# Kernel optimization log

Hardware: AMD Instinct MI355X
Metric: run time of the kernel (lower is better)

The kernel has to match this reference:

```python
import jax, jax.numpy as jnp
import numpy as np
from jax import lax

B, J, C, K, TOK, CH, H = 2048, 17, 480, 3, 64, 960, 6
HD = C // H  # 80
EPS = 1e-5

def gelu(x):
    return jax.nn.gelu(x, approximate=False)

def layernorm(x, g, b):
    mu = jnp.mean(x, axis=-1, keepdims=True)
    var = jnp.var(x, axis=-1, keepdims=True)
    return (x - mu) * lax.rsqrt(var + EPS) * g + b

def groupnorm(x, g, b, groups=16):
    # x: (B, C, J) -> normalize over (C//groups * J) per group
    n, c, j = x.shape
    xg = x.reshape(n, groups, -1)
    mu = jnp.mean(xg, axis=-1, keepdims=True)
    var = jnp.var(xg, axis=-1, keepdims=True)
    xg = (xg - mu) * lax.rsqrt(var + EPS)
    return xg.reshape(n, c, j) * g[None, :, None] + b[None, :, None]

def dwconv1d(x, w, b, pad):
    # x: (B, C, J), w: (C, 1, Kw) depthwise
    y = lax.conv_general_dilated(x, w, window_strides=(1,), padding=[(pad, pad)],
                                 dimension_numbers=('NCH', 'OIH', 'NCH'),
                                 feature_group_count=x.shape[1])
    return y + b[None, :, None]

def setup_inputs() -> dict:
    key = jax.random.key(0)
    ks = jax.random.split(key, 16)
    n = jax.random.normal
    return {
        'x': n(ks[0], (B, J, C), dtype=jnp.float32),
        'adj': n(ks[1], (K, J, J), dtype=jnp.float32) * 0.1,
        'norm1_g': jnp.ones((J,), jnp.float32), 'norm1_b': jnp.zeros((J,), jnp.float32),
        'gcn1_w': n(ks[2], (C * K, C), jnp.float32) * 0.02, 'gcn1_b': jnp.zeros((C * K,), jnp.float32),
        'dw_w': n(ks[3], (C, 1, 7), jnp.float32) * 0.1, 'dw_b': jnp.zeros((C,), jnp.float32),
        'dwgn_g': jnp.ones((C,), jnp.float32), 'dwgn_b': jnp.zeros((C,), jnp.float32),
        'mlp1_w1': n(ks[4], (TOK, J), jnp.float32) * 0.02, 'mlp1_b1': jnp.zeros((TOK,), jnp.float32),
        'mlp1_w2': n(ks[5], (J, TOK), jnp.float32) * 0.02, 'mlp1_b2': jnp.zeros((J,), jnp.float32),
        'qkv_w': n(ks[6], (3 * C, C), jnp.float32) * 0.02, 'qkv_b': jnp.zeros((3 * C,), jnp.float32),
        'proj_w': n(ks[7], (C, C), jnp.float32) * 0.02, 'proj_b': jnp.zeros((C,), jnp.float32),
        'pos_w': n(ks[8], (C, 1, 9), jnp.float32) * 0.1, 'pos_b': jnp.zeros((C,), jnp.float32),
        'gnf_g': jnp.ones((C,), jnp.float32), 'gnf_b': jnp.zeros((C,), jnp.float32),
        'norm2_g': jnp.ones((C,), jnp.float32), 'norm2_b': jnp.zeros((C,), jnp.float32),
        'gcn2_w': n(ks[9], (C * K, C), jnp.float32) * 0.02, 'gcn2_b': jnp.zeros((C * K,), jnp.float32),
        'mlp2_w1': n(ks[10], (CH, C), jnp.float32) * 0.02, 'mlp2_b1': jnp.zeros((CH,), jnp.float32),
        'mlp2_w2': n(ks[11], (C, CH), jnp.float32) * 0.02, 'mlp2_b2': jnp.zeros((C,), jnp.float32),
    }

def reference(x, adj, norm1_g, norm1_b, gcn1_w, gcn1_b, dw_w, dw_b, dwgn_g, dwgn_b,
              mlp1_w1, mlp1_b1, mlp1_w2, mlp1_b2, qkv_w, qkv_b, proj_w, proj_b,
              pos_w, pos_b, gnf_g, gnf_b, norm2_g, norm2_b, gcn2_w, gcn2_b,
              mlp2_w1, mlp2_b1, mlp2_w2, mlp2_b2):
    b = x.shape[0]
    xc = jnp.transpose(x, (0, 2, 1))            # (b, c, j)
    res_spatial = xc
    xn = layernorm(xc, norm1_g, norm1_b)        # LN over joints
    # --- GCN branch 1: 1x1 conv then adjacency einsum ---
    y = jnp.einsum('bcj,oc->boj', xn, gcn1_w) + gcn1_b[None, :, None]
    y = y.reshape(b, K, C, J)
    x_gcn1 = jnp.einsum('bkcv,kvw->bcw', y, adj)  # (b, c, j)
    # --- depthwise conv + GN + GELU + token Mlp ---
    d = gelu(groupnorm(dwconv1d(xn, dw_w, dw_b, 3), dwgn_g, dwgn_b))
    x_mjem = gelu(d @ mlp1_w1.T + mlp1_b1) @ mlp1_w2.T + mlp1_b2  # mix over j
    # --- spatial global attention (6 heads over joints + dwconv pos) ---
    xt = jnp.transpose(xn, (0, 2, 1))           # (b, j, c)
    qkv = xt @ qkv_w.T + qkv_b                  # (b, j, 3c)
    qkv = qkv.reshape(b, J, 3, H, HD).transpose(2, 0, 3, 1, 4)  # (3, b, h, j, hd)
    q, k, v = qkv[0], qkv[1], qkv[2]
    attn = jax.nn.softmax(jnp.einsum('bhqd,bhkd->bhqk', q, k) * (HD ** -0.5), axis=-1)
    o = jnp.einsum('bhqk,bhkd->bhqd', attn, v).transpose(0, 2, 1, 3).reshape(b, J, C)
    o = o @ proj_w.T + proj_b
    x_gsa = jnp.transpose(o, (0, 2, 1)) + dwconv1d(xn, pos_w, pos_b, 4)  # (b, c, j)
    # --- fuse ---
    fused = groupnorm(x_gsa + x_gcn1 + x_mjem, gnf_g, gnf_b)
    xc = res_spatial + gelu(fused)
    # --- channel stage ---
    xj = jnp.transpose(xc, (0, 2, 1))           # (b, j, c)
    res_channel = xj
    xn2 = layernorm(xj, norm2_g, norm2_b)       # LN over channels
    xcc = jnp.transpose(xn2, (0, 2, 1))         # (b, c, j)
    y2 = jnp.einsum('bcj,oc->boj', xcc, gcn2_w) + gcn2_b[None, :, None]
    y2 = y2.reshape(b, K, C, J)
    x_gcn2 = jnp.transpose(jnp.einsum('bkcv,kvw->bcw', y2, adj), (0, 2, 1))  # (b, j, c)
    mlp_out = gelu(xn2 @ mlp2_w1.T + mlp2_b1) @ mlp2_w2.T + mlp2_b2
    # sca_block is undefined in the source __init__ -> identity
    return res_channel + mlp_out + x_gcn2
```

## Files before the change

kernel.cpp:

```cpp
#include <hip/hip_runtime.h>
#include <hip/hip_bf16.h>

#define DI __device__ __forceinline__

typedef __attribute__((ext_vector_type(8))) short bf16x8;
typedef __attribute__((ext_vector_type(4))) float f32x4;

namespace {
constexpr int B_ = 2048, J_ = 17, C_ = 480, K_ = 3, TOK_ = 64, CH_ = 960, H_ = 6, HD_ = 80;
constexpr int C3_ = 3 * C_;
constexpr float EPSF = 1e-5f;
}

DI float gelu_f(float x) {
  const float kA2 = 2.f * 0.7978845608028654f;
  const float kB2 = 2.f * 0.7978845608028654f * 0.044715f;
  const float z = fmaf(-kB2 * x, x * x, -kA2 * x);
  return x / (1.f + __expf(z));
}
DI float b2f(__hip_bfloat16 v) { return __bfloat162float(v); }
DI __hip_bfloat16 f2b(float v) { return __float2bfloat16(v); }
DI float s2f(short s) { return __uint_as_float(((unsigned)(unsigned short)s) << 16); }
DI unsigned pk2(float a, float b) {
  union { unsigned u; __hip_bfloat16 h[2]; } p;
  p.h[0] = f2b(a); p.h[1] = f2b(b);
  return p.u;
}

DI void gl16(const void* g, void* l) {
  __builtin_amdgcn_global_load_lds(
      (const __attribute__((address_space(1))) unsigned int*)g,
      (__attribute__((address_space(3))) unsigned int*)l, 16, 0, 0);
}

__global__ __launch_bounds__(256) void cvt_all_kernel(
    const float* __restrict__ s0, const float* __restrict__ s1,
    const float* __restrict__ s2, const float* __restrict__ s3,
    const float* __restrict__ s4, const float* __restrict__ s5,
    __hip_bfloat16* __restrict__ d) {
  constexpr int SG = C3_ * C_;
  constexpr int O1 = SG, O2 = 2 * SG, O3 = 3 * SG;
  constexpr int O4 = O3 + C_ * C_;
  constexpr int O5 = O4 + CH_ * C_;
  const int i = (blockIdx.x * 256 + threadIdx.x) * 4;
  const float* s; int off;
  if      (i < O1) { s = s0; off = i; }
  else if (i < O2) { s = s1; off = i - O1; }
  else if (i < O3) { s = s2; off = i - O2; }
  else if (i < O4) { s = s3; off = i - O3; }
  else if (i < O5) { s = s4; off = i - O4; }
  else             { s = s5; off = i - O5; }
  const float4 v = *reinterpret_cast<const float4*>(s + off);
  union { ushort4 u; __hip_bfloat16 h[4]; } o;
  o.h[0] = f2b(v.x); o.h[1] = f2b(v.y); o.h[2] = f2b(v.z); o.h[3] = f2b(v.w);
  *reinterpret_cast<ushort4*>(reinterpret_cast<unsigned short*>(d) + i) = o.u;
}

__global__ __launch_bounds__(256) void ln1_kernel(const float* __restrict__ x,
                                                  const float* __restrict__ g,
                                                  const float* __restrict__ bt,
                                                  __hip_bfloat16* __restrict__ xnT, int nBC) {
  const int t = blockIdx.x * 256 + threadIdx.x;
  if (t >= nBC) return;
  const int b = t / C_, c = t % C_;
  const float* xp = x + (size_t)b * J_ * C_ + c;
  float v[J_];
  float s = 0.f;
  #pragma unroll
  for (int j = 0; j < J_; ++j) { v[j] = xp[j * C_]; s += v[j]; }
  const float mu = s * (1.f / J_);
  float sq = 0.f;
  #pragma unroll
  for (int j = 0; j < J_; ++j) { const float d = v[j] - mu; sq += d * d; }
  const float rs = rsqrtf(sq * (1.f / J_) + EPSF);
  __hip_bfloat16* op = xnT + (size_t)b * J_ * C_ + c;
  #pragma unroll
  for (int j = 0; j < J_; ++j) op[j * C_] = f2b((v[j] - mu) * rs * g[j] + bt[j]);
}

template<int KD, int EPI>
__global__ __launch_bounds__(512) void gemm_lds(const __hip_bfloat16* __restrict__ A,
                                                const __hip_bfloat16* __restrict__ W,
                                                const float* __restrict__ bias,
                                                __hip_bfloat16* __restrict__ Dst, int Ntot,
                                                const __hip_bfloat16* __restrict__ r1,
                                                const __hip_bfloat16* __restrict__ r2,
                                                float* __restrict__ outf) {
  constexpr int NST = (KD + 63) / 64;
  constexpr bool TAIL = (KD % 64) != 0;
  constexpr int ROWB = KD * 2;
  __shared__ __align__(16) char smem[28672];

  const int lane = threadIdx.x & 63;
  const int wid  = threadIdx.x >> 6;
  const int m0g = blockIdx.x * 128;
  const int n0g = blockIdx.y * 96;

  const int srow = lane >> 3;
  const int scbs = ((lane & 7) * 16) ^ ((srow & 7) << 4);
  auto stage = [&](int t) {
    const int kb = t * 128;
    #pragma unroll
    for (int i = wid; i < 28; i += 8) {
      if (i < 16) {
        const int r = i * 8 + srow;
        gl16((const char*)A + (size_t)(m0g + r) * ROWB + kb + scbs, smem + i * 1024);
      } else {
        const int r = (i - 16) * 8 + srow;
        gl16((const char*)W + (size_t)(n0g + r) * ROWB + kb + scbs, smem + 16384 + (i - 16) * 1024);
      }
    }
  };

  const f32x4 zf = {0.f, 0.f, 0.f, 0.f};
  f32x4 acc[2][3];
  #pragma unroll
  for (int mi = 0; mi < 2; ++mi)
    #pragma unroll
    for (int ni = 0; ni < 3; ++ni) acc[mi][ni] = zf;

  const int rA0 = (wid >> 1) * 32 + (lane & 15);
  const int rB0 = (wid & 1) * 48 + (lane & 15);
  const int swz = (lane & 7) << 4;
  const int kq  = (lane >> 4) * 16;

  for (int t = 0; t < NST; ++t) {
    stage(t);
    __syncthreads();
    const int nks = (TAIL && t == NST - 1) ? 1 : 2;
    for (int ks = 0; ks < nks; ++ks) {
      const int cb = (ks * 64 + kq) ^ swz;
      bf16x8 av[2], bv[3];
      #pragma unroll
      for (int mi = 0; mi < 2; ++mi)
        av[mi] = *reinterpret_cast<const bf16x8*>(smem + (rA0 + mi * 16) * 128 + cb);
      #pragma unroll
      for (int ni = 0; ni < 3; ++ni)
        bv[ni] = *reinterpret_cast<const bf16x8*>(smem + 16384 + (rB0 + ni * 16) * 128 + cb);
      #pragma unroll
      for (int mi = 0; mi < 2; ++mi)
        #pragma unroll
        for (int ni = 0; ni < 3; ++ni)
          acc[mi][ni] = __builtin_amdgcn_mfma_f32_16x16x32_bf16(av[mi], bv[ni], acc[mi][ni], 0, 0, 0);
    }
    __syncthreads();
  }

  const int lc0 = (wid & 1) * 48 + (lane & 15);
  const int lr0 = (wid >> 1) * 32 + ((lane >> 4) << 2);
  if (EPI == 2) {
    #pragma unroll
    for (int ni = 0; ni < 3; ++ni) {
      const int col = n0g + lc0 + ni * 16;
      const float bvv = bias[col];
      #pragma unroll
      for (int mi = 0; mi < 2; ++mi) {
        #pragma unroll
        for (int r = 0; r < 4; ++r) {
          const size_t idx = (size_t)(m0g + lr0 + mi * 16 + r) * Ntot + col;
          outf[idx] = acc[mi][ni][r] + bvv + b2f(r1[idx]) + b2f(r2[idx]);
        }
      }
    }
  } else {
    __hip_bfloat16* ct = (__hip_bfloat16*)smem;
    #pragma unroll
    for (int ni = 0; ni < 3; ++ni) {
      const float bvv = bias[n0g + lc0 + ni * 16];
      #pragma unroll
      for (int mi = 0; mi < 2; ++mi) {
        #pragma unroll
        for (int r = 0; r < 4; ++r) {
          float v = acc[mi][ni][r] + bvv;
          if (EPI == 1) v = gelu_f(v);
          ct[(lr0 + mi * 16 + r) * 104 + lc0 + ni * 16] = f2b(v);
        }
      }
    }
    __syncthreads();
    const int tid = threadIdx.x;
    #pragma unroll
    for (int it = 0; it < 3; ++it) {
      const int idx = it * 512 + tid;
      const int row = idx / 12, s = idx - row * 12;
      const uint4 v = *(const uint4*)(smem + row * 208 + s * 16);
      *(uint4*)((char*)Dst + ((size_t)(m0g + row) * Ntot + n0g) * 2 + s * 16) = v;
    }
  }
}

__global__ __launch_bounds__(512) void attn_kernel(const __hip_bfloat16* __restrict__ qkv,
                                                   __hip_bfloat16* __restrict__ o) {
  constexpr int SROW = 1448;
  const int b = blockIdx.x, tid = threadIdx.x;
  __shared__ __align__(16) __hip_bfloat16 sqkv[J_ * SROW];
  __shared__ float S[H_][J_][J_];
  {
    const uint4* src = (const uint4*)(qkv + (size_t)b * J_ * C3_);
    uint4* dst = (uint4*)&sqkv[0];
    for (int i = tid; i < 3060; i += 512) {
      const int j = i / 180, u = i - j * 180;
      dst[j * 181 + u] = src[i];
    }
  }
  __syncthreads();
  for (int i = tid; i < H_ * J_ * J_; i += 512) {
    const int h = i / (J_ * J_), r = i % (J_ * J_), qj = r / J_, kj = r % J_;
    const bf16x8* qp = (const bf16x8*)&sqkv[qj * SROW + h * HD_];
    const bf16x8* kp = (const bf16x8*)&sqkv[kj * SROW + C_ + h * HD_];
    float acc = 0.f;
    #pragma unroll
    for (int d8 = 0; d8 < HD_ / 8; ++d8) {
      const bf16x8 qv = qp[d8], kv = kp[d8];
      #pragma unroll
      for (int t = 0; t < 8; ++t) acc += s2f(qv[t]) * s2f(kv[t]);
    }
    S[h][qj][kj] = acc * 0.11180339887498949f;
  }
  __syncthreads();
  if (tid < H_ * J_) {
    const int h = tid / J_, qj = tid % J_;
    float* row = S[h][qj];
    float m = row[0];
    #pragma unroll
    for (int kk = 1; kk < J_; ++kk) m = fmaxf(m, row[kk]);
    float s = 0.f;
    #pragma unroll
    for (int kk = 0; kk < J_; ++kk) { const float e = __expf(row[kk] - m); row[kk] = e; s += e; }
    const float inv = 1.f / s;
    #pragma unroll
    for (int kk = 0; kk < J_; ++kk) row[kk] *= inv;
  }
  __syncthreads();
  __hip_bfloat16* ob = o + (size_t)b * J_ * C_;
  for (int i = tid; i < J_ * C_; i += 512) {
    const int qj = i / C_, c = i % C_;
    const int h = c / HD_;
    const float* srow = S[h][qj];
    float acc = 0.f;
    #pragma unroll
    for (int kk = 0; kk < J_; ++kk) acc += srow[kk] * b2f(sqkv[kk * SROW + 2 * C_ + c]);
    ob[i] = f2b(acc);
  }
}

__global__ __launch_bounds__(512) void gcn_contract_kernel(const __hip_bfloat16* __restrict__ y,
                                                           const float* __restrict__ adj,
                                                           __hip_bfloat16* __restrict__ g) {
  const int b = blockIdx.x, tid = threadIdx.x;
  __shared__ float adjl[K_ * J_ * J_];
  for (int i = tid; i < K_ * J_ * J_; i += 512) adjl[i] = adj[i];
  __syncthreads();
  const int c = tid;
  if (c < C_) {
    float yv[K_][J_];
    const __hip_bfloat16* yb = y + (size_t)b * J_ * C3_ + c;
    #pragma unroll
    for (int k = 0; k < K_; ++k)
      #pragma unroll
      for (int v = 0; v < J_; ++v)
        yv[k][v] = b2f(yb[(size_t)v * C3_ + k * C_]);
    __hip_bfloat16* gp = g + (size_t)b * J_ * C_ + c;
    #pragma unroll
    for (int w = 0; w < J_; ++w) {
      float acc = 0.f;
      #pragma unroll
      for (int k = 0; k < K_; ++k)
        #pragma unroll
        for (int v = 0; v < J_; ++v)
          acc += yv[k][v] * adjl[(k * J_ + v) * J_ + w];
      gp[w * C_] = f2b(acc);
    }
  }
}

__global__ __launch_bounds__(512) void dwconv_kernel(const __hip_bfloat16* __restrict__ xnT,
    const float* __restrict__ dww, const float* __restrict__ dwb,
    const float* __restrict__ gg, const float* __restrict__ gb,
    __hip_bfloat16* __restrict__ dpr) {
  __shared__ __align__(16) __hip_bfloat16 xl[J_ * C_];
  __shared__ float gstat[16][2];
  const int b = blockIdx.x, tid = threadIdx.x;
  {
    const uint4* src = (const uint4*)(xnT + (size_t)b * J_ * C_);
    uint4* dst = (uint4*)&xl[0];
    for (int i = tid; i < 1020; i += 512) dst[i] = src[i];
  }
  if (tid < 32) gstat[tid >> 1][tid & 1] = 0.f;
  __syncthreads();
  const int c = tid;
  float dv[J_];
  if (c < C_) {
    float xv[J_];
    #pragma unroll
    for (int j = 0; j < J_; ++j) xv[j] = b2f(xl[j * C_ + c]);
    float wv[7];
    #pragma unroll
    for (int t = 0; t < 7; ++t) wv[t] = dww[c * 7 + t];
    const float bias = dwb[c];
    float s = 0.f, sqs = 0.f;
    #pragma unroll
    for (int j = 0; j < J_; ++j) {
      float acc = bias;
      #pragma unroll
      for (int t = 0; t < 7; ++t) {
        const int jj = j - 3 + t;
        if (jj >= 0 && jj < J_) acc = fmaf(xv[jj], wv[t], acc);
      }
      dv[j] = acc; s += acc; sqs += acc * acc;
    }
    atomicAdd(&gstat[c / 30][0], s);
    atomicAdd(&gstat[c / 30][1], sqs);
  }
  __syncthreads();
// ... 55 lines not shown
    #pragma unroll
    for (int kk = 0; kk < 2; ++kk)
      a2[mi][kk] = *(const bf16x8*)(lds + W2P + (lr + mi * 16) * 144 + kk * 64 + kc * 16);
  float b1v[4][4];
  #pragma unroll
  for (int mi = 0; mi < 4; ++mi)
    #pragma unroll
    for (int r = 0; r < 4; ++r) b1v[mi][r] = b1[mi * 16 + kc * 4 + r];
  float b2v[4];
  #pragma unroll
  for (int r = 0; r < 4; ++r) b2v[r] = b2[kc * 4 + r];
  const float b2v16 = b2[16];

  char* hs = lds + HS + wid * 2304;
  const f32x4 zf4 = {0.f, 0.f, 0.f, 0.f};
  #pragma unroll
  for (int it = 0; it < 4; ++it) {
    const int gcb = blockIdx.x * 16 + wid * 4 + it;
    const int b = gcb / 30, cbl = gcb - b * 30;
    const size_t row0 = (size_t)b * C_ + cbl * 16;
    const bf16x8 bf = *(const bf16x8*)(dpr + (row0 + lr) * 32 + kc * 8);
    f32x4 acc1[4];
    #pragma unroll
    for (int mi = 0; mi < 4; ++mi)
      acc1[mi] = __builtin_amdgcn_mfma_f32_16x16x32_bf16(a1[mi], bf, zf4, 0, 0, 0);
    #pragma unroll
    for (int mi = 0; mi < 4; ++mi) {
      const float g0 = gelu_f(acc1[mi][0] + b1v[mi][0]);
      const float g1 = gelu_f(acc1[mi][1] + b1v[mi][1]);
      const float g2 = gelu_f(acc1[mi][2] + b1v[mi][2]);
      const float g3 = gelu_f(acc1[mi][3] + b1v[mi][3]);
      unsigned* hp = (unsigned*)(hs + lr * 144 + (mi * 16 + kc * 4) * 2);
      hp[0] = pk2(g0, g1);
      hp[1] = pk2(g2, g3);
    }
    f32x4 acc2[2] = {zf4, zf4};
    #pragma unroll
    for (int kk = 0; kk < 2; ++kk) {
      const bf16x8 hb = *(const bf16x8*)(hs + lr * 144 + kk * 64 + kc * 16);
      #pragma unroll
      for (int mi = 0; mi < 2; ++mi)
        acc2[mi] = __builtin_amdgcn_mfma_f32_16x16x32_bf16(a2[mi][kk], hb, acc2[mi], 0, 0, 0);
    }
    __hip_bfloat16* mp = mjem_r + (row0 + lr) * 20;
    #pragma unroll
    for (int r = 0; r < 4; ++r)
      mp[kc * 4 + r] = f2b(acc2[0][r] + b2v[r]);
    if (kc == 0) mp[16] = f2b(acc2[1][0] + b2v16);
  }
}

__global__ __launch_bounds__(512) void fuse_kernel(
    const float* __restrict__ x, const __hip_bfloat16* __restrict__ xnT,
    const __hip_bfloat16* __restrict__ g1o, const __hip_bfloat16* __restrict__ projo,
    const __hip_bfloat16* __restrict__ mjem_r,
    const float* __restrict__ posw, const float* __restrict__ posb,
    const float* __restrict__ gnfg, const float* __restrict__ gnfb,
    const float* __restrict__ n2g, const float* __restrict__ n2b,
    __hip_bfloat16* __restrict__ resch, __hip_bfloat16* __restrict__ xn2) {
  const int b = blockIdx.x, tid = threadIdx.x;
  __shared__ float xcl[J_][C_];
  __shared__ float gstat[16][2];
  __shared__ float lnst[J_][2];
  if (tid < 32) gstat[tid >> 1][tid & 1] = 0.f;
  __syncthreads();
  const int c = tid;
  float fz[J_];
  if (c < C_) {
    float xnv[J_];
    const __hip_bfloat16* xp = xnT + (size_t)b * J_ * C_ + c;
    #pragma unroll
    for (int j = 0; j < J_; ++j) xnv[j] = b2f(xp[j * C_]);
    float pw[9];
    #pragma unroll
    for (int t = 0; t < 9; ++t) pw[t] = posw[c * 9 + t];
    const float pb = posb[c];
    const __hip_bfloat16* pj = projo + (size_t)b * J_ * C_ + c;
    const __hip_bfloat16* mp = mjem_r + ((size_t)b * C_ + c) * 20;
    const __hip_bfloat16* gp = g1o + (size_t)b * J_ * C_ + c;
    float s = 0.f, sqs = 0.f;
    #pragma unroll
    for (int j = 0; j < J_; ++j) {
      float pos = pb;
      #pragma unroll
      for (int t = 0; t < 9; ++t) {
        const int jj = j - 4 + t;
        if (jj >= 0 && jj < J_) pos += xnv[jj] * pw[t];
      }
      const float f = b2f(pj[j * C_]) + pos + b2f(gp[j * C_]) + b2f(mp[j]);
      fz[j] = f; s += f; sqs += f * f;
    }
    atomicAdd(&gstat[c / 30][0], s);
    atomicAdd(&gstat[c / 30][1], sqs);
  }
  __syncthreads();
  if (c < C_) {
    const float mu = gstat[c / 30][0] * (1.f / 510.f);
    const float var = gstat[c / 30][1] * (1.f / 510.f) - mu * mu;
    const float rs = rsqrtf(var + EPSF);
    const float sc = gnfg[c], of = gnfb[c];
    const float* xr = x + (size_t)b * J_ * C_ + c;
    __hip_bfloat16* rp = resch + (size_t)b * J_ * C_ + c;
    #pragma unroll
    for (int j = 0; j < J_; ++j) {
      const float xcv = xr[j * C_] + gelu_f((fz[j] - mu) * rs * sc + of);
      xcl[j][c] = xcv;
      rp[j * C_] = f2b(xcv);
    }
  }
  __syncthreads();
  const int wid = tid >> 6, lane = tid & 63;
  for (int j = wid; j < J_; j += 8) {
    float ls = 0.f, lq = 0.f;
    for (int cc = lane; cc < C_; cc += 64) { const float v = xcl[j][cc]; ls += v; lq += v * v; }
    #pragma unroll
    for (int off = 32; off > 0; off >>= 1) { ls += __shfl_xor(ls, off); lq += __shfl_xor(lq, off); }
    if (lane == 0) {
      const float mu = ls * (1.f / C_);
      const float var = lq * (1.f / C_) - mu * mu;
      lnst[j][0] = mu; lnst[j][1] = rsqrtf(var + EPSF);
    }
  }
  __syncthreads();
  if (c < C_) {
    const float sc = n2g[c], of = n2b[c];
    __hip_bfloat16* xp2 = xn2 + (size_t)b * J_ * C_ + c;
    #pragma unroll
    for (int j = 0; j < J_; ++j)
      xp2[j * C_] = f2b((xcl[j][c] - lnst[j][0]) * lnst[j][1] * sc + of);
  }
}

extern "C" void kernel_launch(void* const* d_in, const int* in_sizes, int n_in,
                              void* d_out, int out_size, void* d_ws, size_t ws_size,
                              hipStream_t stream) {
  const float* x      = (const float*)d_in[0];
  const float* adj    = (const float*)d_in[1];
  const float* n1g    = (const float*)d_in[2];
  const float* n1b    = (const float*)d_in[3];
  const float* gcn1_w = (const float*)d_in[4];
  const float* gcn1_b = (const float*)d_in[5];
  const float* dw_w   = (const float*)d_in[6];
  const float* dw_b   = (const float*)d_in[7];
  const float* dwgn_g = (const float*)d_in[8];
  const float* dwgn_b = (const float*)d_in[9];
  const float* m1w1   = (const float*)d_in[10];
  const float* m1b1   = (const float*)d_in[11];
  const float* m1w2   = (const float*)d_in[12];
  const float* m1b2   = (const float*)d_in[13];
  const float* qkv_w  = (const float*)d_in[14];
  const float* qkv_b  = (const float*)d_in[15];
  const float* proj_w = (const float*)d_in[16];
  const float* proj_b = (const float*)d_in[17];
  const float* pos_w  = (const float*)d_in[18];
  const float* pos_b  = (const float*)d_in[19];
  const float* gnf_g  = (const float*)d_in[20];
  const float* gnf_b  = (const float*)d_in[21];
  const float* n2g    = (const float*)d_in[22];
  const float* n2b    = (const float*)d_in[23];
  const float* gcn2_w = (const float*)d_in[24];
  const float* gcn2_b = (const float*)d_in[25];
  const float* m2w1   = (const float*)d_in[26];
  const float* m2b1   = (const float*)d_in[27];
  const float* m2w2   = (const float*)d_in[28];
  const float* m2b2   = (const float*)d_in[29];
  float* out = (float*)d_out;
  char* ws = (char*)d_ws;
  (void)in_sizes; (void)n_in; (void)out_size;

  auto a256 = [](size_t b) { return (b + 255) & ~(size_t)255; };
  const size_t wbytes = 3 * a256((size_t)C3_ * C_ * 2) + a256((size_t)C_ * C_ * 2) +
                        a256((size_t)CH_ * C_ * 2) + a256((size_t)C_ * CH_ * 2);
  int nch = 16;
  for (int cand : {1, 2, 4, 8, 16}) {
    const size_t Bcb = (size_t)(B_ / cand);
    const size_t Mcb = Bcb * J_;
    const size_t fp = wbytes + a256(Mcb * C3_ * 2) + 5 * a256(Mcb * C_ * 2) +
                      a256(Bcb * C_ * 20 * 2) + a256(Bcb * C_ * 32 * 2);
    if (fp <= ws_size) { nch = cand; break; }
  }
  const int Bc = B_ / nch;
  const int Mc = Bc * J_;

  size_t off = 0;
  auto alloc = [&](size_t bytes) { char* p = ws + off; off += a256(bytes); return p; };
  __hip_bfloat16* w_qkv = (__hip_bfloat16*)alloc((size_t)C3_ * C_ * 2);
  __hip_bfloat16* w_g1  = (__hip_bfloat16*)alloc((size_t)C3_ * C_ * 2);
  __hip_bfloat16* w_g2  = (__hip_bfloat16*)alloc((size_t)C3_ * C_ * 2);
  __hip_bfloat16* w_pr  = (__hip_bfloat16*)alloc((size_t)C_ * C_ * 2);
  __hip_bfloat16* w_21  = (__hip_bfloat16*)alloc((size_t)CH_ * C_ * 2);
  __hip_bfloat16* w_22  = (__hip_bfloat16*)alloc((size_t)C_ * CH_ * 2);
  __hip_bfloat16* BIG   = (__hip_bfloat16*)alloc((size_t)Mc * C3_ * 2);
  __hip_bfloat16* xnT   = (__hip_bfloat16*)alloc((size_t)Mc * C_ * 2);
  __hip_bfloat16* attno = (__hip_bfloat16*)alloc((size_t)Mc * C_ * 2);
  __hip_bfloat16* projo = (__hip_bfloat16*)alloc((size_t)Mc * C_ * 2);
  __hip_bfloat16* g1o   = (__hip_bfloat16*)alloc((size_t)Mc * C_ * 2);
  __hip_bfloat16* resch = (__hip_bfloat16*)alloc((size_t)Mc * C_ * 2);
  __hip_bfloat16* mjemr = (__hip_bfloat16*)alloc((size_t)Bc * C_ * 20 * 2);
  __hip_bfloat16* dpr   = (__hip_bfloat16*)alloc((size_t)Bc * C_ * 32 * 2);
  __hip_bfloat16* xn2   = attno;
  __hip_bfloat16* g2o   = g1o;
  __hip_bfloat16* hbuf  = BIG;

  cvt_all_kernel<<<3150, 256, 0, stream>>>(qkv_w, gcn1_w, gcn2_w, proj_w, m2w1, m2w2, w_qkv);

  for (int ci = 0; ci < nch; ++ci) {
    const float* xc = x + (size_t)ci * Bc * J_ * C_;
    float* outc = out + (size_t)ci * Bc * J_ * C_;
    ln1_kernel<<<(Bc * C_ + 255) / 256, 256, 0, stream>>>(xc, n1g, n1b, xnT, Bc * C_);
    gemm_lds<C_, 0><<<dim3(Mc / 128, C3_ / 96), 512, 0, stream>>>(xnT, w_qkv, qkv_b, BIG, C3_, nullptr, nullptr, nullptr);
    attn_kernel<<<Bc, 512, 0, stream>>>(BIG, attno);
    gemm_lds<C_, 0><<<dim3(Mc / 128, C3_ / 96), 512, 0, stream>>>(xnT, w_g1, gcn1_b, BIG, C3_, nullptr, nullptr, nullptr);
    gcn_contract_kernel<<<Bc, 512, 0, stream>>>(BIG, adj, g1o);
    gemm_lds<C_, 0><<<dim3(Mc / 128, C_ / 96), 512, 0, stream>>>(attno, w_pr, proj_b, projo, C_, nullptr, nullptr, nullptr);
    dwconv_kernel<<<Bc, 512, 0, stream>>>(xnT, dw_w, dw_b, dwgn_g, dwgn_b, dpr);
    mlp_kernel<<<Bc * 30 / 16, 256, 0, stream>>>(dpr, m1w1, m1b1, m1w2, m1b2, mjemr);
    fuse_kernel<<<Bc, 512, 0, stream>>>(xc, xnT, g1o, projo, mjemr, pos_w, pos_b,
                                        gnf_g, gnf_b, n2g, n2b, resch, xn2);
    gemm_lds<C_, 0><<<dim3(Mc / 128, C3_ / 96), 512, 0, stream>>>(xn2, w_g2, gcn2_b, BIG, C3_, nullptr, nullptr, nullptr);
    gcn_contract_kernel<<<Bc, 512, 0, stream>>>(BIG, adj, g2o);
    gemm_lds<C_, 1><<<dim3(Mc / 128, CH_ / 96), 512, 0, stream>>>(xn2, w_21, m2b1, hbuf, CH_, nullptr, nullptr, nullptr);
    gemm_lds<CH_, 2><<<dim3(Mc / 128, C_ / 96), 512, 0, stream>>>(hbuf, w_22, m2b2, nullptr, C_, resch, g2o, outc);
  }
}
```

Before: 735.4 us.

## Switch GEMM tiles to 128x128 with padded N dimensions

Changes the GEMM block tile from 128x96 to 128x128, giving each wave a 4x2 MFMA subtile. Weights and intermediate buffers are zero-padded to multiples of 128 columns (1536, 1024, 512), and the consumer kernels are updated to the new strides. This improves operand reuse per LDS read and reduces A-tile refetch across blocks. The cost is extra padded MFMA work and a larger LDS footprint.

```diff
diff --git a/kernel.cpp b/kernel.cpp
--- a/kernel.cpp
+++ b/kernel.cpp
@@ -9,6 +9,7 @@
 namespace {
 constexpr int B_ = 2048, J_ = 17, C_ = 480, K_ = 3, TOK_ = 64, CH_ = 960, H_ = 6, HD_ = 80;
 constexpr int C3_ = 3 * C_;
+constexpr int C3P_ = 1536, CHP_ = 1024, CP_ = 512;
 constexpr float EPSF = 1e-5f;
 }
 
@@ -33,26 +34,20 @@
       (__attribute__((address_space(3))) unsigned int*)l, 16, 0, 0);
 }
 
-__global__ __launch_bounds__(256) void cvt_all_kernel(
-    const float* __restrict__ s0, const float* __restrict__ s1,
-    const float* __restrict__ s2, const float* __restrict__ s3,
-    const float* __restrict__ s4, const float* __restrict__ s5,
-    __hip_bfloat16* __restrict__ d) {
-  constexpr int SG = C3_ * C_;
-  constexpr int O1 = SG, O2 = 2 * SG, O3 = 3 * SG;
-  constexpr int O4 = O3 + C_ * C_;
-  constexpr int O5 = O4 + CH_ * C_;
-  const int i = (blockIdx.x * 256 + threadIdx.x) * 4;
-  const float* s; int off;
-  if      (i < O1) { s = s0; off = i; }
-  else if (i < O2) { s = s1; off = i - O1; }
-  else if (i < O3) { s = s2; off = i - O2; }
-  else if (i < O4) { s = s3; off = i - O3; }
-  else if (i < O5) { s = s4; off = i - O4; }
-  else             { s = s5; off = i - O5; }
-  const float4 v = *reinterpret_cast<const float4*>(s + off);
+__global__ __launch_bounds__(256) void cvt_pad_kernel(const float* __restrict__ s,
+                                                      __hip_bfloat16* __restrict__ d,
+                                                      int Nlog, int Kd, int n4) {
+  const int q = blockIdx.x * 256 + threadIdx.x;
+  if (q >= n4) return;
+  const int i = q * 4;
+  const int row = i / Kd, col = i - row * Kd;
   union { ushort4 u; __hip_bfloat16 h[4]; } o;
-  o.h[0] = f2b(v.x); o.h[1] = f2b(v.y); o.h[2] = f2b(v.z); o.h[3] = f2b(v.w);
+  if (row < Nlog) {
+    const float4 v = *reinterpret_cast<const float4*>(s + (size_t)row * Kd + col);
+    o.h[0] = f2b(v.x); o.h[1] = f2b(v.y); o.h[2] = f2b(v.z); o.h[3] = f2b(v.w);
+  } else {
+    o.h[0] = f2b(0.f); o.h[1] = f2b(0.f); o.h[2] = f2b(0.f); o.h[3] = f2b(0.f);
+  }
   *reinterpret_cast<ushort4*>(reinterpret_cast<unsigned short*>(d) + i) = o.u;
 }
 
@@ -78,49 +73,51 @@
   for (int j = 0; j < J_; ++j) op[j * C_] = f2b((v[j] - mu) * rs * g[j] + bt[j]);
 }
 
-template<int KD, int EPI>
+template<int KD, int LDA, int EPI>
 __global__ __launch_bounds__(512) void gemm_lds(const __hip_bfloat16* __restrict__ A,
                                                 const __hip_bfloat16* __restrict__ W,
                                                 const float* __restrict__ bias,
-                                                __hip_bfloat16* __restrict__ Dst, int Ntot,
+                                                __hip_bfloat16* __restrict__ Dst,
+                                                int NP, int Nlog,
                                                 const __hip_bfloat16* __restrict__ r1,
                                                 const __hip_bfloat16* __restrict__ r2,
                                                 float* __restrict__ outf) {
   constexpr int NST = (KD + 63) / 64;
   constexpr bool TAIL = (KD % 64) != 0;
-  constexpr int ROWB = KD * 2;
-  __shared__ __align__(16) char smem[28672];
+  constexpr int AROWB = LDA * 2;
+  constexpr int WROWB = KD * 2;
+  __shared__ __align__(16) char smem[34816];
 
   const int lane = threadIdx.x & 63;
   const int wid  = threadIdx.x >> 6;
   const int m0g = blockIdx.x * 128;
-  const int n0g = blockIdx.y * 96;
+  const int n0g = blockIdx.y * 128;
 
   const int srow = lane >> 3;
   const int scbs = ((lane & 7) * 16) ^ ((srow & 7) << 4);
   auto stage = [&](int t) {
     const int kb = t * 128;
     #pragma unroll
-    for (int i = wid; i < 28; i += 8) {
+    for (int i = wid; i < 32; i += 8) {
       if (i < 16) {
         const int r = i * 8 + srow;
-        gl16((const char*)A + (size_t)(m0g + r) * ROWB + kb + scbs, smem + i * 1024);
+        gl16((const char*)A + (size_t)(m0g + r) * AROWB + kb + scbs, smem + i * 1024);
       } else {
         const int r = (i - 16) * 8 + srow;
-        gl16((const char*)W + (size_t)(n0g + r) * ROWB + kb + scbs, smem + 16384 + (i - 16) * 1024);
+        gl16((const char*)W + (size_t)(n0g + r) * WROWB + kb + scbs, smem + 16384 + (i - 16) * 1024);
       }
     }
   };
 
   const f32x4 zf = {0.f, 0.f, 0.f, 0.f};
-  f32x4 acc[2][3];
-  #pragma unroll
-  for (int mi = 0; mi < 2; ++mi)
-    #pragma unroll
-    for (int ni = 0; ni < 3; ++ni) acc[mi][ni] = zf;
-
-  const int rA0 = (wid >> 1) * 32 + (lane & 15);
-  const int rB0 = (wid & 1) * 48 + (lane & 15);
+  f32x4 acc[4][2];
+  #pragma unroll
+  for (int mi = 0; mi < 4; ++mi)
+    #pragma unroll
+    for (int ni = 0; ni < 2; ++ni) acc[mi][ni] = zf;
+
+  const int rA0 = (wid >> 2) * 64 + (lane & 15);
+  const int rB0 = (wid & 3) * 32 + (lane & 15);
   const int swz = (lane & 7) << 4;
   const int kq  = (lane >> 4) * 16;
 
@@ -130,61 +127,64 @@
     const int nks = (TAIL && t == NST - 1) ? 1 : 2;
     for (int ks = 0; ks < nks; ++ks) {
       const int cb = (ks * 64 + kq) ^ swz;
-      bf16x8 av[2], bv[3];
-      #pragma unroll
-      for (int mi = 0; mi < 2; ++mi)
+      bf16x8 av[4], bv[2];
+      #pragma unroll
+      for (int mi = 0; mi < 4; ++mi)
         av[mi] = *reinterpret_cast<const bf16x8*>(smem + (rA0 + mi * 16) * 128 + cb);
       #pragma unroll
-      for (int ni = 0; ni < 3; ++ni)
+      for (int ni = 0; ni < 2; ++ni)
         bv[ni] = *reinterpret_cast<const bf16x8*>(smem + 16384 + (rB0 + ni * 16) * 128 + cb);
       #pragma unroll
-      for (int mi = 0; mi < 2; ++mi)
+      for (int mi = 0; mi < 4; ++mi)
         #pragma unroll
-        for (int ni = 0; ni < 3; ++ni)
+        for (int ni = 0; ni < 2; ++ni)
           acc[mi][ni] = __builtin_amdgcn_mfma_f32_16x16x32_bf16(av[mi], bv[ni], acc[mi][ni], 0, 0, 0);
     }
     __syncthreads();
   }
 
-  const int lc0 = (wid & 1) * 48 + (lane & 15);
-  const int lr0 = (wid >> 1) * 32 + ((lane >> 4) << 2);
+  const int lc0 = (wid & 3) * 32 + (lane & 15);
+  const int lr0 = (wid >> 2) * 64 + ((lane >> 4) << 2);
   if (EPI == 2) {
     #pragma unroll
-    for (int ni = 0; ni < 3; ++ni) {
+    for (int ni = 0; ni < 2; ++ni) {
       const int col = n0g + lc0 + ni * 16;
-      const float bvv = bias[col];
-      #pragma unroll
-      for (int mi = 0; mi < 2; ++mi) {
+      if (col < Nlog) {
+        const float bvv = bias[col];
         #pragma unroll
-        for (int r = 0; r < 4; ++r) {
-          const size_t idx = (size_t)(m0g + lr0 + mi * 16 + r) * Ntot + col;
-          outf[idx] = acc[mi][ni][r] + bvv + b2f(r1[idx]) + b2f(r2[idx]);
+        for (int mi = 0; mi < 4; ++mi) {
+          #pragma unroll
+          for (int r = 0; r < 4; ++r) {
+            const size_t idx = (size_t)(m0g + lr0 + mi * 16 + r) * Nlog + col;
+            outf[idx] = acc[mi][ni][r] + bvv + b2f(r1[idx]) + b2f(r2[idx]);
+          }
         }
       }
     }
   } else {
     __hip_bfloat16* ct = (__hip_bfloat16*)smem;
     #pragma unroll
-    for (int ni = 0; ni < 3; ++ni) {
-      const float bvv = bias[n0g + lc0 + ni * 16];
-      #pragma unroll
-      for (int mi = 0; mi < 2; ++mi) {
+    for (int ni = 0; ni < 2; ++ni) {
+      const int col = n0g + lc0 + ni * 16;
+      const float bvv = (col < Nlog) ? bias[col] : 0.f;
+      #pragma unroll
+      for (int mi = 0; mi < 4; ++mi) {
         #pragma unroll
         for (int r = 0; r < 4; ++r) {
           float v = acc[mi][ni][r] + bvv;
           if (EPI == 1) v = gelu_f(v);
-          ct[(lr0 + mi * 16 + r) * 104 + lc0 + ni * 16] = f2b(v);
+          ct[(lr0 + mi * 16 + r) * 136 + lc0 + ni * 16] = f2b(v);
         }
       }
     }
     __syncthreads();
     const int tid = threadIdx.x;
     #pragma unroll
-    for (int it = 0; it < 3; ++it) {
+    for (int it = 0; it < 4; ++it) {
       const int idx = it * 512 + tid;
-      const int row = idx / 12, s = idx - row * 12;
-      const uint4 v = *(const uint4*)(smem + row * 208 + s * 16);
-      *(uint4*)((char*)Dst + ((size_t)(m0g + row) * Ntot + n0g) * 2 + s * 16) = v;
+      const int row = idx >> 4, s = idx & 15;
+      const uint4 v = *(const uint4*)(smem + row * 272 + s * 16);
+      *(uint4*)((char*)Dst + ((size_t)(m0g + row) * NP + n0g) * 2 + s * 16) = v;
     }
   }
 }
@@ -196,11 +196,11 @@
   __shared__ __align__(16) __hip_bfloat16 sqkv[J_ * SROW];
   __shared__ float S[H_][J_][J_];
   {
-    const uint4* src = (const uint4*)(qkv + (size_t)b * J_ * C3_);
+    const uint4* src = (const uint4*)(qkv + (size_t)b * J_ * C3P_);
     uint4* dst = (uint4*)&sqkv[0];
     for (int i = tid; i < 3060; i += 512) {
       const int j = i / 180, u = i - j * 180;
-      dst[j * 181 + u] = src[i];
+      dst[j * 181 + u] = src[j * 192 + u];
     }
   }
   __syncthreads();
@@ -254,12 +254,12 @@
   const int c = tid;
   if (c < C_) {
     float yv[K_][J_];
-    const __hip_bfloat16* yb = y + (size_t)b * J_ * C3_ + c;
+    const __hip_bfloat16* yb = y + (size_t)b * J_ * C3P_ + c;
     #pragma unroll
     for (int k = 0; k < K_; ++k)
       #pragma unroll
       for (int v = 0; v < J_; ++v)
-        yv[k][v] = b2f(yb[(size_t)v * C3_ + k * C_]);
+        yv[k][v] = b2f(yb[(size_t)v * C3P_ + k * C_]);
     __hip_bfloat16* gp = g + (size_t)b * J_ * C_ + c;
     #pragma unroll
     for (int w = 0; w < J_; ++w) {
@@ -444,7 +444,7 @@
     #pragma unroll
     for (int t = 0; t < 9; ++t) pw[t] = posw[c * 9 + t];
     const float pb = posb[c];
-    const __hip_bfloat16* pj = projo + (size_t)b * J_ * C_ + c;
+    const __hip_bfloat16* pj = projo + (size_t)b * J_ * CP_ + c;
     const __hip_bfloat16* mp = mjem_r + ((size_t)b * C_ + c) * 20;
     const __hip_bfloat16* gp = g1o + (size_t)b * J_ * C_ + c;
     float s = 0.f, sqs = 0.f;
@@ -456,7 +456,7 @@
         const int jj = j - 4 + t;
         if (jj >= 0 && jj < J_) pos += xnv[jj] * pw[t];
       }
-      const float f = b2f(pj[j * C_]) + pos + b2f(gp[j * C_]) + b2f(mp[j]);
+      const float f = b2f(pj[j * CP_]) + pos + b2f(gp[j * C_]) + b2f(mp[j]);
       fz[j] = f; s += f; sqs += f * f;
     }
     atomicAdd(&gstat[c / 30][0], s);
@@ -538,13 +538,14 @@
   (void)in_sizes; (void)n_in; (void)out_size;
 
   auto a256 = [](size_t b) { return (b + 255) & ~(size_t)255; };
-  const size_t wbytes = 3 * a256((size_t)C3_ * C_ * 2) + a256((size_t)C_ * C_ * 2) +
-                        a256((size_t)CH_ * C_ * 2) + a256((size_t)C_ * CH_ * 2);
+  const size_t wbytes = 3 * a256((size_t)C3P_ * C_ * 2) + a256((size_t)CP_ * C_ * 2) +
+                        a256((size_t)CHP_ * C_ * 2) + a256((size_t)CP_ * CH_ * 2);
   int nch = 16;
   for (int cand : {1, 2, 4, 8, 16}) {
     const size_t Bcb = (size_t)(B_ / cand);
     const size_t Mcb = Bcb * J_;
-    const size_t fp = wbytes + a256(Mcb * C3_ * 2) + 5 * a256(Mcb * C_ * 2) +
+    const size_t fp = wbytes + a256(Mcb * C3P_ * 2) + a256(Mcb * CP_ * 2) +
+                      4 * a256(Mcb * C_ * 2) +
                       a256(Bcb * C_ * 20 * 2) + a256(Bcb * C_ * 32 * 2);
     if (fp <= ws_size) { nch = cand; break; }
   }
@@ -553,16 +554,16 @@
 
   size_t off = 0;
   auto alloc = [&](size_t bytes) { char* p = ws + off; off += a256(bytes); return p; };
-  __hip_bfloat16* w_qkv = (__hip_bfloat16*)alloc((size_t)C3_ * C_ * 2);
-  __hip_bfloat16* w_g1  = (__hip_bfloat16*)alloc((size_t)C3_ * C_ * 2);
-  __hip_bfloat16* w_g2  = (__hip_bfloat16*)alloc((size_t)C3_ * C_ * 2);
-  __hip_bfloat16* w_pr  = (__hip_bfloat16*)alloc((size_t)C_ * C_ * 2);
-  __hip_bfloat16* w_21  = (__hip_bfloat16*)alloc((size_t)CH_ * C_ * 2);
-  __hip_bfloat16* w_22  = (__hip_bfloat16*)alloc((size_t)C_ * CH_ * 2);
-  __hip_bfloat16* BIG   = (__hip_bfloat16*)alloc((size_t)Mc * C3_ * 2);
+  __hip_bfloat16* w_qkv = (__hip_bfloat16*)alloc((size_t)C3P_ * C_ * 2);
+  __hip_bfloat16* w_g1  = (__hip_bfloat16*)alloc((size_t)C3P_ * C_ * 2);
+  __hip_bfloat16* w_g2  = (__hip_bfloat16*)alloc((size_t)C3P_ * C_ * 2);
+  __hip_bfloat16* w_pr  = (__hip_bfloat16*)alloc((size_t)CP_ * C_ * 2);
+  __hip_bfloat16* w_21  = (__hip_bfloat16*)alloc((size_t)CHP_ * C_ * 2);
+  __hip_bfloat16* w_22  = (__hip_bfloat16*)alloc((size_t)CP_ * CH_ * 2);
+  __hip_bfloat16* BIG   = (__hip_bfloat16*)alloc((size_t)Mc * C3P_ * 2);
+  __hip_bfloat16* projo = (__hip_bfloat16*)alloc((size_t)Mc * CP_ * 2);
   __hip_bfloat16* xnT   = (__hip_bfloat16*)alloc((size_t)Mc * C_ * 2);
   __hip_bfloat16* attno = (__hip_bfloat16*)alloc((size_t)Mc * C_ * 2);
-  __hip_bfloat16* projo = (__hip_bfloat16*)alloc((size_t)Mc * C_ * 2);
   __hip_bfloat16* g1o   = (__hip_bfloat16*)alloc((size_t)Mc * C_ * 2);
   __hip_bfloat16* resch = (__hip_bfloat16*)alloc((size_t)Mc * C_ * 2);
   __hip_bfloat16* mjemr = (__hip_bfloat16*)alloc((size_t)Bc * C_ * 20 * 2);
@@ -571,24 +572,33 @@
   __hip_bfloat16* g2o   = g1o;
   __hip_bfloat16* hbuf  = BIG;
 
-  cvt_all_kernel<<<3150, 256, 0, stream>>>(qkv_w, gcn1_w, gcn2_w, proj_w, m2w1, m2w2, w_qkv);
+  auto cvtp = [&](const float* s, __hip_bfloat16* d, int Nlog, int NP, int Kd) {
+    const int n4 = NP * Kd / 4;
+    cvt_pad_kernel<<<(n4 + 255) / 256, 256, 0, stream>>>(s, d, Nlog, Kd, n4);
+  };
+  cvtp(qkv_w,  w_qkv, C3_, C3P_, C_);
+  cvtp(gcn1_w, w_g1,  C3_, C3P_, C_);
+  cvtp(gcn2_w, w_g2,  C3_, C3P_, C_);
+  cvtp(proj_w, w_pr,  C_,  CP_,  C_);
+  cvtp(m2w1,   w_21,  CH_, CHP_, C_);
+  cvtp(m2w2,   w_22,  C_,  CP_,  CH_);
 
   for (int ci = 0; ci < nch; ++ci) {
     const float* xc = x + (size_t)ci * Bc * J_ * C_;
     float* outc = out + (size_t)ci * Bc * J_ * C_;
     ln1_kernel<<<(Bc * C_ + 255) / 256, 256, 0, stream>>>(xc, n1g, n1b, xnT, Bc * C_);
-    gemm_lds<C_, 0><<<dim3(Mc / 128, C3_ / 96), 512, 0, stream>>>(xnT, w_qkv, qkv_b, BIG, C3_, nullptr, nullptr, nullptr);
+    gemm_lds<C_, C_, 0><<<dim3(Mc / 128, C3P_ / 128), 512, 0, stream>>>(xnT, w_qkv, qkv_b, BIG, C3P_, C3_, nullptr, nullptr, nullptr);
     attn_kernel<<<Bc, 512, 0, stream>>>(BIG, attno);
-    gemm_lds<C_, 0><<<dim3(Mc / 128, C3_ / 96), 512, 0, stream>>>(xnT, w_g1, gcn1_b, BIG, C3_, nullptr, nullptr, nullptr);
+    gemm_lds<C_, C_, 0><<<dim3(Mc / 128, C3P_ / 128), 512, 0, stream>>>(xnT, w_g1, gcn1_b, BIG, C3P_, C3_, nullptr, nullptr, nullptr);
     gcn_contract_kernel<<<Bc, 512, 0, stream>>>(BIG, adj, g1o);
-    gemm_lds<C_, 0><<<dim3(Mc / 128, C_ / 96), 512, 0, stream>>>(attno, w_pr, proj_b, projo, C_, nullptr, nullptr, nullptr);
+    gemm_lds<C_, C_, 0><<<dim3(Mc / 128, CP_ / 128), 512, 0, stream>>>(attno, w_pr, proj_b, projo, CP_, C_, nullptr, nullptr, nullptr);
     dwconv_kernel<<<Bc, 512, 0, stream>>>(xnT, dw_w, dw_b, dwgn_g, dwgn_b, dpr);
     mlp_kernel<<<Bc * 30 / 16, 256, 0, stream>>>(dpr, m1w1, m1b1, m1w2, m1b2, mjemr);
     fuse_kernel<<<Bc, 512, 0, stream>>>(xc, xnT, g1o, projo, mjemr, pos_w, pos_b,
                                         gnf_g, gnf_b, n2g, n2b, resch, xn2);
-    gemm_lds<C_, 0><<<dim3(Mc / 128, C3_ / 96), 512, 0, stream>>>(xn2, w_g2, gcn2_b, BIG, C3_, nullptr, nullptr, nullptr);
+    gemm_lds<C_, C_, 0><<<dim3(Mc / 128, C3P_ / 128), 512, 0, stream>>>(xn2, w_g2, gcn2_b, BIG, C3P_, C3_, nullptr, nullptr, nullptr);
     gcn_contract_kernel<<<Bc, 512, 0, stream>>>(BIG, adj, g2o);
-    gemm_lds<C_, 1><<<dim3(Mc / 128, CH_ / 96), 512, 0, stream>>>(xn2, w_21, m2b1, hbuf, CH_, nullptr, nullptr, nullptr);
-    gemm_lds<CH_, 2><<<dim3(Mc / 128, C_ / 96), 512, 0, stream>>>(hbuf, w_22, m2b2, nullptr, C_, resch, g2o, outc);
-  }
-}
+    gemm_lds<C_, C_, 1><<<dim3(Mc / 128, CHP_ / 128), 512, 0, stream>>>(xn2, w_21, m2b1, hbuf, CHP_, CH_, nullptr, nullptr, nullptr);
+    gemm_lds<CH_, CHP_, 2><<<dim3(Mc / 128, CP_ / 128), 512, 0, stream>>>(hbuf, w_22, m2b2, nullptr, CP_, C_, resch, g2o, outc);
+  }
+}
```

After: 791.1 us. 1.08x slower.

## Merge QKV and GCN1 GEMMs, fuse GCN1 contraction into fuse kernel, XCD-aware tile mapping

Applied to the files above, without the earlier changes.

The QKV and GCN1 projections now run as one GEMM with N=2880 over a shared input, relying on w_g1 sitting directly after w_qkv in the workspace and on a split bias lookup. The GCN1 adjacency contraction moves into the fuse kernel, so the separate gcn_contract launch and the g1o round trip through memory go away. GEMMs switch to a 1D grid with an XCD-aware block-id remap to improve L2 locality across the chiplets. The cost is a larger intermediate buffer, which may force more batch chunks, plus extra per-thread work and register pressure in the fuse kernel.

```diff
diff --git a/kernel.cpp b/kernel.cpp
--- a/kernel.cpp
+++ b/kernel.cpp
@@ -9,6 +9,7 @@
 namespace {
 constexpr int B_ = 2048, J_ = 17, C_ = 480, K_ = 3, TOK_ = 64, CH_ = 960, H_ = 6, HD_ = 80;
 constexpr int C3_ = 3 * C_;
+constexpr int NM_ = 2880;
 constexpr float EPSF = 1e-5f;
 }
 
@@ -81,8 +82,9 @@
 template<int KD, int EPI>
 __global__ __launch_bounds__(512) void gemm_lds(const __hip_bfloat16* __restrict__ A,
                                                 const __hip_bfloat16* __restrict__ W,
-                                                const float* __restrict__ bias,
-                                                __hip_bfloat16* __restrict__ Dst, int Ntot,
+                                                const float* __restrict__ bias1,
+                                                const float* __restrict__ bias2, int bsplit,
+                                                __hip_bfloat16* __restrict__ Dst, int Ntot, int nM,
                                                 const __hip_bfloat16* __restrict__ r1,
                                                 const __hip_bfloat16* __restrict__ r2,
                                                 float* __restrict__ outf) {
@@ -91,11 +93,15 @@
   constexpr int ROWB = KD * 2;
   __shared__ __align__(16) char smem[28672];
 
+  const int nwg = gridDim.x, id = blockIdx.x;
+  const int q = nwg >> 3, r = nwg & 7;
+  const int xcd = id & 7, ii = id >> 3;
+  const int sid = (xcd < r ? xcd * (q + 1) : r * (q + 1) + (xcd - r) * q) + ii;
+  const int m0g = (sid % nM) * 128;
+  const int n0g = (sid / nM) * 96;
+
   const int lane = threadIdx.x & 63;
   const int wid  = threadIdx.x >> 6;
-  const int m0g = blockIdx.x * 128;
-  const int n0g = blockIdx.y * 96;
-
   const int srow = lane >> 3;
   const int scbs = ((lane & 7) * 16) ^ ((srow & 7) << 4);
   auto stage = [&](int t) {
@@ -103,11 +109,11 @@
     #pragma unroll
     for (int i = wid; i < 28; i += 8) {
       if (i < 16) {
-        const int r = i * 8 + srow;
-        gl16((const char*)A + (size_t)(m0g + r) * ROWB + kb + scbs, smem + i * 1024);
+        const int rr = i * 8 + srow;
+        gl16((const char*)A + (size_t)(m0g + rr) * ROWB + kb + scbs, smem + i * 1024);
       } else {
-        const int r = (i - 16) * 8 + srow;
-        gl16((const char*)W + (size_t)(n0g + r) * ROWB + kb + scbs, smem + 16384 + (i - 16) * 1024);
+        const int rr = (i - 16) * 8 + srow;
+        gl16((const char*)W + (size_t)(n0g + rr) * ROWB + kb + scbs, smem + 16384 + (i - 16) * 1024);
       }
     }
   };
@@ -152,13 +158,13 @@
     #pragma unroll
     for (int ni = 0; ni < 3; ++ni) {
       const int col = n0g + lc0 + ni * 16;
-      const float bvv = bias[col];
+      const float bvv = (col < bsplit) ? bias1[col] : bias2[col - bsplit];
       #pragma unroll
       for (int mi = 0; mi < 2; ++mi) {
         #pragma unroll
-        for (int r = 0; r < 4; ++r) {
-          const size_t idx = (size_t)(m0g + lr0 + mi * 16 + r) * Ntot + col;
-          outf[idx] = acc[mi][ni][r] + bvv + b2f(r1[idx]) + b2f(r2[idx]);
+        for (int r4 = 0; r4 < 4; ++r4) {
+          const size_t idx = (size_t)(m0g + lr0 + mi * 16 + r4) * Ntot + col;
+          outf[idx] = acc[mi][ni][r4] + bvv + b2f(r1[idx]) + b2f(r2[idx]);
         }
       }
     }
@@ -166,14 +172,15 @@
     __hip_bfloat16* ct = (__hip_bfloat16*)smem;
     #pragma unroll
     for (int ni = 0; ni < 3; ++ni) {
-      const float bvv = bias[n0g + lc0 + ni * 16];
+      const int col = n0g + lc0 + ni * 16;
+      const float bvv = (col < bsplit) ? bias1[col] : bias2[col - bsplit];
       #pragma unroll
       for (int mi = 0; mi < 2; ++mi) {
         #pragma unroll
-        for (int r = 0; r < 4; ++r) {
-          float v = acc[mi][ni][r] + bvv;
+        for (int r4 = 0; r4 < 4; ++r4) {
+          float v = acc[mi][ni][r4] + bvv;
           if (EPI == 1) v = gelu_f(v);
-          ct[(lr0 + mi * 16 + r) * 104 + lc0 + ni * 16] = f2b(v);
+          ct[(lr0 + mi * 16 + r4) * 104 + lc0 + ni * 16] = f2b(v);
         }
       }
     }
@@ -196,11 +203,11 @@
   __shared__ __align__(16) __hip_bfloat16 sqkv[J_ * SROW];
   __shared__ float S[H_][J_][J_];
   {
-    const uint4* src = (const uint4*)(qkv + (size_t)b * J_ * C3_);
+    const uint4* src = (const uint4*)(qkv + (size_t)b * J_ * NM_);
     uint4* dst = (uint4*)&sqkv[0];
     for (int i = tid; i < 3060; i += 512) {
       const int j = i / 180, u = i - j * 180;
-      dst[j * 181 + u] = src[i];
+      dst[j * 181 + u] = src[j * 360 + u];
     }
   }
   __syncthreads();
@@ -246,7 +253,8 @@
 
 __global__ __launch_bounds__(512) void gcn_contract_kernel(const __hip_bfloat16* __restrict__ y,
                                                            const float* __restrict__ adj,
-                                                           __hip_bfloat16* __restrict__ g) {
+                                                           __hip_bfloat16* __restrict__ g,
+                                                           int ldy, int offy) {
   const int b = blockIdx.x, tid = threadIdx.x;
   __shared__ float adjl[K_ * J_ * J_];
   for (int i = tid; i < K_ * J_ * J_; i += 512) adjl[i] = adj[i];
@@ -254,12 +262,12 @@
   const int c = tid;
   if (c < C_) {
     float yv[K_][J_];
-    const __hip_bfloat16* yb = y + (size_t)b * J_ * C3_ + c;
+    const __hip_bfloat16* yb = y + (size_t)b * J_ * ldy + offy + c;
     #pragma unroll
     for (int k = 0; k < K_; ++k)
       #pragma unroll
       for (int v = 0; v < J_; ++v)
-        yv[k][v] = b2f(yb[(size_t)v * C3_ + k * C_]);
+        yv[k][v] = b2f(yb[(size_t)v * ldy + k * C_]);
     __hip_bfloat16* gp = g + (size_t)b * J_ * C_ + c;
     #pragma unroll
     for (int w = 0; w < J_; ++w) {
@@ -421,16 +429,18 @@
 
 __global__ __launch_bounds__(512) void fuse_kernel(
     const float* __restrict__ x, const __hip_bfloat16* __restrict__ xnT,
-    const __hip_bfloat16* __restrict__ g1o, const __hip_bfloat16* __restrict__ projo,
-    const __hip_bfloat16* __restrict__ mjem_r,
+    const __hip_bfloat16* __restrict__ y1, const float* __restrict__ adj,
+    const __hip_bfloat16* __restrict__ projo, const __hip_bfloat16* __restrict__ mjem_r,
     const float* __restrict__ posw, const float* __restrict__ posb,
     const float* __restrict__ gnfg, const float* __restrict__ gnfb,
     const float* __restrict__ n2g, const float* __restrict__ n2b,
     __hip_bfloat16* __restrict__ resch, __hip_bfloat16* __restrict__ xn2) {
   const int b = blockIdx.x, tid = threadIdx.x;
   __shared__ float xcl[J_][C_];
+  __shared__ float adjl[K_ * J_ * J_];
   __shared__ float gstat[16][2];
   __shared__ float lnst[J_][2];
+  for (int i = tid; i < K_ * J_ * J_; i += 512) adjl[i] = adj[i];
   if (tid < 32) gstat[tid >> 1][tid & 1] = 0.f;
   __syncthreads();
   const int c = tid;
@@ -446,8 +456,6 @@
     const float pb = posb[c];
     const __hip_bfloat16* pj = projo + (size_t)b * J_ * C_ + c;
     const __hip_bfloat16* mp = mjem_r + ((size_t)b * C_ + c) * 20;
-    const __hip_bfloat16* gp = g1o + (size_t)b * J_ * C_ + c;
-    float s = 0.f, sqs = 0.f;
     #pragma unroll
     for (int j = 0; j < J_; ++j) {
       float pos = pb;
@@ -456,9 +464,25 @@
         const int jj = j - 4 + t;
         if (jj >= 0 && jj < J_) pos += xnv[jj] * pw[t];
       }
-      const float f = b2f(pj[j * C_]) + pos + b2f(gp[j * C_]) + b2f(mp[j]);
-      fz[j] = f; s += f; sqs += f * f;
-    }
+      fz[j] = b2f(pj[j * C_]) + pos + b2f(mp[j]);
+    }
+    const __hip_bfloat16* yb = y1 + (size_t)b * J_ * NM_ + C3_ + c;
+    #pragma unroll
+    for (int k = 0; k < K_; ++k) {
+      float yv[J_];
+      #pragma unroll
+      for (int v = 0; v < J_; ++v) yv[v] = b2f(yb[(size_t)v * NM_ + k * C_]);
+      #pragma unroll
+      for (int j = 0; j < J_; ++j) {
+        float acc = 0.f;
+        #pragma unroll
+        for (int v = 0; v < J_; ++v) acc = fmaf(yv[v], adjl[(k * J_ + v) * J_ + j], acc);
+        fz[j] += acc;
+      }
+    }
+    float s = 0.f, sqs = 0.f;
+    #pragma unroll
+    for (int j = 0; j < J_; ++j) { s += fz[j]; sqs += fz[j] * fz[j]; }
     atomicAdd(&gstat[c / 30][0], s);
     atomicAdd(&gstat[c / 30][1], sqs);
   }
@@ -544,12 +568,13 @@
   for (int cand : {1, 2, 4, 8, 16}) {
     const size_t Bcb = (size_t)(B_ / cand);
     const size_t Mcb = Bcb * J_;
-    const size_t fp = wbytes + a256(Mcb * C3_ * 2) + 5 * a256(Mcb * C_ * 2) +
+    const size_t fp = wbytes + a256(Mcb * NM_ * 2) + 5 * a256(Mcb * C_ * 2) +
                       a256(Bcb * C_ * 20 * 2) + a256(Bcb * C_ * 32 * 2);
     if (fp <= ws_size) { nch = cand; break; }
   }
   const int Bc = B_ / nch;
   const int Mc = Bc * J_;
+  const int nMB = Mc / 128;
 
   size_t off = 0;
   auto alloc = [&](size_t bytes) { char* p = ws + off; off += a256(bytes); return p; };
@@ -559,17 +584,17 @@
   __hip_bfloat16* w_pr  = (__hip_bfloat16*)alloc((size_t)C_ * C_ * 2);
   __hip_bfloat16* w_21  = (__hip_bfloat16*)alloc((size_t)CH_ * C_ * 2);
   __hip_bfloat16* w_22  = (__hip_bfloat16*)alloc((size_t)C_ * CH_ * 2);
-  __hip_bfloat16* BIG   = (__hip_bfloat16*)alloc((size_t)Mc * C3_ * 2);
+  __hip_bfloat16* BIG   = (__hip_bfloat16*)alloc((size_t)Mc * NM_ * 2);
   __hip_bfloat16* xnT   = (__hip_bfloat16*)alloc((size_t)Mc * C_ * 2);
   __hip_bfloat16* attno = (__hip_bfloat16*)alloc((size_t)Mc * C_ * 2);
   __hip_bfloat16* projo = (__hip_bfloat16*)alloc((size_t)Mc * C_ * 2);
-  __hip_bfloat16* g1o   = (__hip_bfloat16*)alloc((size_t)Mc * C_ * 2);
+  __hip_bfloat16* g2o   = (__hip_bfloat16*)alloc((size_t)Mc * C_ * 2);
   __hip_bfloat16* resch = (__hip_bfloat16*)alloc((size_t)Mc * C_ * 2);
   __hip_bfloat16* mjemr = (__hip_bfloat16*)alloc((size_t)Bc * C_ * 20 * 2);
   __hip_bfloat16* dpr   = (__hip_bfloat16*)alloc((size_t)Bc * C_ * 32 * 2);
   __hip_bfloat16* xn2   = attno;
-  __hip_bfloat16* g2o   = g1o;
   __hip_bfloat16* hbuf  = BIG;
+  (void)w_g1;
 
   cvt_all_kernel<<<3150, 256, 0, stream>>>(qkv_w, gcn1_w, gcn2_w, proj_w, m2w1, m2w2, w_qkv);
 
@@ -577,18 +602,21 @@
     const float* xc = x + (size_t)ci * Bc * J_ * C_;
     float* outc = out + (size_t)ci * Bc * J_ * C_;
     ln1_kernel<<<(Bc * C_ + 255) / 256, 256, 0, stream>>>(xc, n1g, n1b, xnT, Bc * C_);
-    gemm_lds<C_, 0><<<dim3(Mc / 128, C3_ / 96), 512, 0, stream>>>(xnT, w_qkv, qkv_b, BIG, C3_, nullptr, nullptr, nullptr);
+    gemm_lds<C_, 0><<<nMB * (NM_ / 96), 512, 0, stream>>>(xnT, w_qkv, qkv_b, gcn1_b, C3_,
+                                                          BIG, NM_, nMB, nullptr, nullptr, nullptr);
     attn_kernel<<<Bc, 512, 0, stream>>>(BIG, attno);
-    gemm_lds<C_, 0><<<dim3(Mc / 128, C3_ / 96), 512, 0, stream>>>(xnT, w_g1, gcn1_b, BIG, C3_, nullptr, nullptr, nullptr);
-    gcn_contract_kernel<<<Bc, 512, 0, stream>>>(BIG, adj, g1o);
-    gemm_lds<C_, 0><<<dim3(Mc / 128, C_ / 96), 512, 0, stream>>>(attno, w_pr, proj_b, projo, C_, nullptr, nullptr, nullptr);
+    gemm_lds<C_, 0><<<nMB * (C_ / 96), 512, 0, stream>>>(attno, w_pr, proj_b, proj_b, C_,
+                                                         projo, C_, nMB, nullptr, nullptr, nullptr);
     dwconv_kernel<<<Bc, 512, 0, stream>>>(xnT, dw_w, dw_b, dwgn_g, dwgn_b, dpr);
     mlp_kernel<<<Bc * 30 / 16, 256, 0, stream>>>(dpr, m1w1, m1b1, m1w2, m1b2, mjemr);
-    fuse_kernel<<<Bc, 512, 0, stream>>>(xc, xnT, g1o, projo, mjemr, pos_w, pos_b,
+    fuse_kernel<<<Bc, 512, 0, stream>>>(xc, xnT, BIG, adj, projo, mjemr, pos_w, pos_b,
                                         gnf_g, gnf_b, n2g, n2b, resch, xn2);
-    gemm_lds<C_, 0><<<dim3(Mc / 128, C3_ / 96), 512, 0, stream>>>(xn2, w_g2, gcn2_b, BIG, C3_, nullptr, nullptr, nullptr);
-    gcn_contract_kernel<<<Bc, 512, 0, stream>>>(BIG, adj, g2o);
-    gemm_lds<C_, 1><<<dim3(Mc / 128, CH_ / 96), 512, 0, stream>>>(xn2, w_21, m2b1, hbuf, CH_, nullptr, nullptr, nullptr);
-    gemm_lds<CH_, 2><<<dim3(Mc / 128, C_ / 96), 512, 0, stream>>>(hbuf, w_22, m2b2, nullptr, C_, resch, g2o, outc);
-  }
-}
+    gemm_lds<C_, 0><<<nMB * (C3_ / 96), 512, 0, stream>>>(xn2, w_g2, gcn2_b, gcn2_b, C3_,
+                                                          BIG, C3_, nMB, nullptr, nullptr, nullptr);
+    gcn_contract_kernel<<<Bc, 512, 0, stream>>>(BIG, adj, g2o, C3_, 0);
+    gemm_lds<C_, 1><<<nMB * (CH_ / 96), 512, 0, stream>>>(xn2, w_21, m2b1, m2b1, CH_,
+                                                          hbuf, CH_, nMB, nullptr, nullptr, nullptr);
+    gemm_lds<CH_, 2><<<nMB * (C_ / 96), 512, 0, stream>>>(hbuf, w_22, m2b2, m2b2, C_,
+                                                          nullptr, C_, nMB, resch, g2o, outc);
+  }
+}
```

New measurement: 919.1 us. 1.25x slower.
